# Performance work log

Measured on AMD Instinct MI355X. Metric: run time of the kernel, lower is better.

## Reference

```python
import jax, jax.numpy as jnp
import numpy as np

N = 50000   # nodes
E = 800000  # edges (avg degree 16)
IN, H, OUT = 128, 128, 64


def setup_inputs() -> dict:
    key = jax.random.key(0)
    ks = jax.random.split(key, 8)

    def w(k, shape):
        fan_in = shape[0]
        return (jax.random.normal(k, shape, jnp.float32) / np.float32(np.sqrt(fan_in)))

    x = jax.random.normal(ks[0], (N, IN), jnp.float32)
    edge_index = jax.random.randint(ks[1], (2, E), 0, N, jnp.int64)
    return {
        "x": x,
        "edge_index": edge_index,
        "W1": w(ks[2], (IN, H)), "b1": jnp.zeros((H,), jnp.float32),
        "W2": w(ks[3], (H, H)),  "b2": jnp.zeros((H,), jnp.float32),
        "W3": w(ks[4], (H, H)),  "b3": jnp.zeros((H,), jnp.float32),
        "Wd1": w(ks[5], (H, H)), "bd1": jnp.zeros((H,), jnp.float32),
        "Wd2": w(ks[6], (H, OUT)), "bd2": jnp.zeros((OUT,), jnp.float32),
    }


def _gcn_conv(x, src, dst, norm, W, b):
    # x: [N, Cin] -> linear transform, gather along edges, normalized scatter-add
    h = x @ W                                   # [N, Cout]
    msg = h[src] * norm[:, None]                # [E+N, Cout]
    out = jax.ops.segment_sum(msg, dst, num_segments=N)
    return out + b


def reference(x, edge_index, W1, b1, W2, b2, W3, b3, Wd1, bd1, Wd2, bd2):
    # Add self-loops (PyG GCNConv default) and compute symmetric normalization.
    loops = jnp.arange(N, dtype=edge_index.dtype)
    src = jnp.concatenate([edge_index[0], loops])   # [E+N]
    dst = jnp.concatenate([edge_index[1], loops])   # [E+N]
    deg = jax.ops.segment_sum(jnp.ones_like(dst, dtype=x.dtype), dst, num_segments=N)
    dinv = jnp.where(deg > 0, jax.lax.rsqrt(deg), jnp.zeros_like(deg))
    norm = dinv[src] * dinv[dst]                    # [E+N]

    h = jax.nn.relu(_gcn_conv(x, src, dst, norm, W1, b1))
    h = jax.nn.relu(_gcn_conv(h, src, dst, norm, W2, b2))
    h = jax.nn.relu(_gcn_conv(h, src, dst, norm, W3, b3))

    h = jax.nn.relu(h @ Wd1 + bd1)
    return jax.nn.sigmoid(h @ Wd2 + bd2)            # [N, OUT]
```

## Files before the change

kernel.cpp:

```cpp
#include <hip/hip_runtime.h>
#include <hip/hip_bf16.h>
#include <hip/hip_fp16.h>

#define N_NODES 50000
#define N_EDGES 800000
#define C_H 128
#define C_OUT 64
#define NBLK 196
#define TSTRIDE 136
#define E_PAD 950272
#define MM_BLKS 782

typedef __attribute__((ext_vector_type(8))) short bf16x8;
typedef __attribute__((ext_vector_type(4))) float f32x4;

static __device__ __forceinline__ float bf_lo(unsigned int u) { return __uint_as_float(u << 16); }
static __device__ __forceinline__ float bf_hi(unsigned int u) { return __uint_as_float(u & 0xffff0000u); }
static __device__ __forceinline__ unsigned short f2bf(float f) {
    __hip_bfloat16 h = __float2bfloat16(f);
    return *(unsigned short*)&h;
}
static __device__ __forceinline__ unsigned int pack2(float a, float b) {
    return (unsigned int)f2bf(a) | ((unsigned int)f2bf(b) << 16);
}
static __device__ __forceinline__ unsigned short f2h_bits(float f) {
    union { __half h; unsigned short u; } c; c.h = __float2half_rn(f); return c.u;
}
static __device__ __forceinline__ float h_bits2f(unsigned short u) {
    union { __half h; unsigned short u; } c; c.u = u; return __half2float(c.h);
}

__global__ void prep_kernel(const int* __restrict__ dst, int* __restrict__ counts,
                            int* __restrict__ rank,
                            const float* __restrict__ W1, const float* __restrict__ W2,
                            const float* __restrict__ W3, const float* __restrict__ Wd1,
                            const float* __restrict__ Wd2,
                            unsigned short* __restrict__ P1, unsigned short* __restrict__ P2,
                            unsigned short* __restrict__ P3, unsigned short* __restrict__ Pd1,
                            unsigned short* __restrict__ Pd2,
                            unsigned int* __restrict__ epay) {
    int b = blockIdx.x;
    if (b < 3125) {
        int e = b * 256 + threadIdx.x;
        rank[e] = atomicAdd(&counts[dst[e]], 1);
    } else if (b < 3413) {
        int idx = (b - 3125) * 256 + threadIdx.x;
        if (idx < 4 * 16384) {
            int which = idx >> 14;
            int r = idx & 16383;
            const float* W = (which == 0) ? W1 : (which == 1) ? W2 : (which == 2) ? W3 : Wd1;
            unsigned short* P = (which == 0) ? P1 : (which == 1) ? P2 : (which == 2) ? P3 : Pd1;
            int j = r & 7, lane = (r >> 3) & 63, t = r >> 9;
            int nb = t & 7, kb = t >> 3;
            int k = kb * 32 + ((lane >> 4) << 3) + j;
            int n = nb * 16 + (lane & 15);
            P[r] = f2bf(W[(size_t)k * 128 + n]);
        } else {
            int r = idx - 65536;
            if (r < 8192) {
                int j = r & 7, lane = (r >> 3) & 63, t = r >> 9;
                int nb = t & 3, kb = t >> 2;
                int k = kb * 32 + ((lane >> 4) << 3) + j;
                int n = nb * 16 + (lane & 15);
                Pd2[r] = f2bf(Wd2[(size_t)k * 64 + n]);
            }
        }
    } else {
        int i = (b - 3413) * 256 + threadIdx.x;
        *(uint4*)(epay + (size_t)i * 4) = make_uint4(0, 0, 0, 0);
    }
}

__global__ void __launch_bounds__(256) scan1_kernel(const int* __restrict__ counts,
                                                    int* __restrict__ eblk,
                                                    int* __restrict__ bsum,
                                                    float* __restrict__ dinv) {
    __shared__ int ws[4];
    int i = blockIdx.x * 256 + threadIdx.x;
    int v = (i < N_NODES) ? counts[i] : 0;
    if (i < N_NODES) dinv[i] = rsqrtf((float)v + 1.0f);
    int vp = (v + 3) & ~3;
    int lane = threadIdx.x & 63, w = threadIdx.x >> 6;
    int x = vp;
    #pragma unroll
    for (int off = 1; off < 64; off <<= 1) {
        int t = __shfl_up(x, off, 64);
        if (lane >= off) x += t;
    }
    if (lane == 63) ws[w] = x;
    __syncthreads();
    if (threadIdx.x == 0) {
        int run = 0;
        #pragma unroll
        for (int k = 0; k < 4; ++k) { int t = ws[k]; ws[k] = run; run += t; }
        bsum[blockIdx.x] = run;
    }
    __syncthreads();
    if (i < N_NODES) eblk[i] = x - vp + ws[w];
}

__global__ void __launch_bounds__(256) scan2_kernel(const int* __restrict__ bsum,
                                                    int* __restrict__ bo,
                                                    int* __restrict__ rowptr) {
    __shared__ int ws[4];
    int i = threadIdx.x;
    int v = (i < NBLK) ? bsum[i] : 0;
    int lane = i & 63, w = i >> 6;
    int x = v;
    #pragma unroll
    for (int off = 1; off < 64; off <<= 1) {
        int t = __shfl_up(x, off, 64);
        if (lane >= off) x += t;
    }
    if (lane == 63) ws[w] = x;
    __syncthreads();
    if (i == 0) {
        int run = 0;
        #pragma unroll
        for (int k = 0; k < 4; ++k) { int t = ws[k]; ws[k] = run; run += t; }
    }
    __syncthreads();
    int excl = x - v + ws[w];
    if (i < NBLK) bo[i] = excl;
    if (i == 255) rowptr[N_NODES] = excl + v;
}

__global__ void scan3_kernel(const int* __restrict__ eblk, const int* __restrict__ bo,
                             int* __restrict__ rowptr) {
    int i = blockIdx.x * 256 + threadIdx.x;
    if (i < N_NODES) rowptr[i] = eblk[i] + bo[blockIdx.x];
}

__global__ void __launch_bounds__(256) fill_mm_kernel(
        const float* __restrict__ x, const unsigned short* __restrict__ P1,
        unsigned short* __restrict__ XW1,
        const int* __restrict__ src, const int* __restrict__ dst,
        const float* __restrict__ dinv,
        const int* __restrict__ rowptr, const int* __restrict__ rank,
        unsigned int* __restrict__ epay) {
    int b = blockIdx.x;
    if (b < MM_BLKS) {
        const int lane = threadIdx.x & 63;
        const int wave = threadIdx.x >> 6;
        const int wid  = b * 4 + wave;
        if (wid * 16 >= N_NODES) return;
        const int node = wid * 16 + (lane & 15);
        const int quad = lane >> 4;
        f32x4 acc[8];
        #pragma unroll
        for (int nb = 0; nb < 8; ++nb) acc[nb] = (f32x4){0.f, 0.f, 0.f, 0.f};
        #pragma unroll
        for (int kb = 0; kb < 4; ++kb) {
            const float* p = x + (size_t)node * 128 + kb * 32 + quad * 8;
            float4 lo = *(const float4*)p;
            float4 hi = *(const float4*)(p + 4);
            union { bf16x8 v; unsigned int u[4]; } tmp;
            tmp.u[0] = pack2(lo.x, lo.y); tmp.u[1] = pack2(lo.z, lo.w);
            tmp.u[2] = pack2(hi.x, hi.y); tmp.u[3] = pack2(hi.z, hi.w);
            #pragma unroll
            for (int nb = 0; nb < 8; ++nb) {
                bf16x8 wf = *(const bf16x8*)(P1 + ((size_t)(kb * 8 + nb) * 64 + lane) * 8);
                acc[nb] = __builtin_amdgcn_mfma_f32_16x16x32_bf16(wf, tmp.v, acc[nb], 0, 0, 0);
            }
        }
        #pragma unroll
        for (int nb = 0; nb < 8; ++nb) {
            int ch = nb * 16 + quad * 4;
            uint2 o;
            o.x = pack2(acc[nb][0], acc[nb][1]);
            o.y = pack2(acc[nb][2], acc[nb][3]);
            *(uint2*)(XW1 + (size_t)node * C_H + ch) = o;
        }
    } else {
        int e = (b - MM_BLKS) * 256 + threadIdx.x;
        if (e < N_EDGES) {
            int d = dst[e], s = src[e];
            int pos = rowptr[d] + rank[e];
            float nrm = dinv[s] * dinv[d];
            epay[pos] = (unsigned int)s | ((unsigned int)f2h_bits(nrm) << 16);
        }
    }
}

__global__ void __launch_bounds__(256) gather1_kernel(
        const int* __restrict__ rowptr,
        const unsigned int* __restrict__ epay,
        const float* __restrict__ dinv,
        const unsigned short* __restrict__ hin,
        const float* __restrict__ bias,
        unsigned short* __restrict__ out) {
    int t    = blockIdx.x * 256 + threadIdx.x;
    int node = t >> 4;
    int c8   = (t & 15) << 3;

    float di = dinv[node], dii = di * di;
    uint4 raw = *(const uint4*)(hin + (size_t)node * C_H + c8);
    float a0 = bf_lo(raw.x) * dii, a1 = bf_hi(raw.x) * dii;
    float a2 = bf_lo(raw.y) * dii, a3 = bf_hi(raw.y) * dii;
    float a4 = bf_lo(raw.z) * dii, a5 = bf_hi(raw.z) * dii;
    float a6 = bf_lo(raw.w) * dii, a7 = bf_hi(raw.w) * dii;
    int beg = rowptr[node], end = rowptr[node + 1];
    int p = beg;
    for (; p + 8 <= end; p += 8) {
        uint4 ev0 = *(const uint4*)(epay + p);
        uint4 ev1 = *(const uint4*)(epay + p + 4);
        unsigned int ee[8] = {ev0.x, ev0.y, ev0.z, ev0.w, ev1.x, ev1.y, ev1.z, ev1.w};
        uint4 rv[8];
        #pragma unroll
        for (int j = 0; j < 8; ++j)
            rv[j] = *(const uint4*)(hin + (size_t)(ee[j] & 0xffffu) * C_H + c8);
        #pragma unroll
        for (int j = 0; j < 8; ++j) {
            float nm = h_bits2f((unsigned short)(ee[j] >> 16));
            a0 = fmaf(bf_lo(rv[j].x), nm, a0); a1 = fmaf(bf_hi(rv[j].x), nm, a1);
            a2 = fmaf(bf_lo(rv[j].y), nm, a2); a3 = fmaf(bf_hi(rv[j].y), nm, a3);
            a4 = fmaf(bf_lo(rv[j].z), nm, a4); a5 = fmaf(bf_hi(rv[j].z), nm, a5);
            a6 = fmaf(bf_lo(rv[j].w), nm, a6); a7 = fmaf(bf_hi(rv[j].w), nm, a7);
        }
    }
    if (p < end) {
        uint4 ev = *(const uint4*)(epay + p);
        unsigned int ee[4] = {ev.x, ev.y, ev.z, ev.w};
        uint4 rv[4];
        #pragma unroll
        for (int j = 0; j < 4; ++j)
            rv[j] = *(const uint4*)(hin + (size_t)(ee[j] & 0xffffu) * C_H + c8);
        #pragma unroll
        for (int j = 0; j < 4; ++j) {
            float nm = h_bits2f((unsigned short)(ee[j] >> 16));
            a0 = fmaf(bf_lo(rv[j].x), nm, a0); a1 = fmaf(bf_hi(rv[j].x), nm, a1);
            a2 = fmaf(bf_lo(rv[j].y), nm, a2); a3 = fmaf(bf_hi(rv[j].y), nm, a3);
            a4 = fmaf(bf_lo(rv[j].z), nm, a4); a5 = fmaf(bf_hi(rv[j].z), nm, a5);
            a6 = fmaf(bf_lo(rv[j].w), nm, a6); a7 = fmaf(bf_hi(rv[j].w), nm, a7);
        }
    }
    float4 ba = *(const float4*)(bias + c8);
    float4 bb = *(const float4*)(bias + c8 + 4);
    a0 = fmaxf(a0 + ba.x, 0.f); a1 = fmaxf(a1 + ba.y, 0.f);
    a2 = fmaxf(a2 + ba.z, 0.f); a3 = fmaxf(a3 + ba.w, 0.f);
    a4 = fmaxf(a4 + bb.x, 0.f); a5 = fmaxf(a5 + bb.y, 0.f);
    a6 = fmaxf(a6 + bb.z, 0.f); a7 = fmaxf(a7 + bb.w, 0.f);
    uint4 o;
    o.x = pack2(a0, a1); o.y = pack2(a2, a3);
    o.z = pack2(a4, a5); o.w = pack2(a6, a7);
    *(uint4*)(out + (size_t)node * C_H + c8) = o;
}

template <bool FINAL>
__global__ void __launch_bounds__(256) fused_layer_kernel(
        const int* __restrict__ rowptr,
        const unsigned int* __restrict__ epay,
        const float* __restrict__ dinv,
        const unsigned short* __restrict__ hin,
        const unsigned short* __restrict__ Wp,
        const float* __restrict__ bias,
        const unsigned short* __restrict__ Wd1p,
        const float* __restrict__ bd1,
        const unsigned short* __restrict__ Wd2p,
        const float* __restrict__ bd2,
        unsigned short* __restrict__ out_b,
        float* __restrict__ out_f) {
    __shared__ unsigned short sG[16 * TSTRIDE];
    const int t = threadIdx.x;

    {
        int nl = t >> 4, c8 = (t & 15) << 3;
        int node = blockIdx.x * 16 + nl;
        float di = dinv[node], dii = di * di;
        uint4 raw = *(const uint4*)(hin + (size_t)node * C_H + c8);
        float a0 = bf_lo(raw.x) * dii, a1 = bf_hi(raw.x) * dii;
        float a2 = bf_lo(raw.y) * dii, a3 = bf_hi(raw.y) * dii;
        float a4 = bf_lo(raw.z) * dii, a5 = bf_hi(raw.z) * dii;
        float a6 = bf_lo(raw.w) * dii, a7 = bf_hi(raw.w) * dii;
        int beg = rowptr[node], end = rowptr[node + 1];
        int p = beg;
        for (; p + 8 <= end; p += 8) {
            uint4 ev0 = *(const uint4*)(epay + p);
            uint4 ev1 = *(const uint4*)(epay + p + 4);
            unsigned int ee[8] = {ev0.x, ev0.y, ev0.z, ev0.w, ev1.x, ev1.y, ev1.z, ev1.w};
            uint4 rv[8];
            #pragma unroll
            for (int j = 0; j < 8; ++j)
                rv[j] = *(const uint4*)(hin + (size_t)(ee[j] & 0xffffu) * C_H + c8);
            #pragma unroll
            for (int j = 0; j < 8; ++j) {
                float nm = h_bits2f((unsigned short)(ee[j] >> 16));
                a0 = fmaf(bf_lo(rv[j].x), nm, a0); a1 = fmaf(bf_hi(rv[j].x), nm, a1);
                a2 = fmaf(bf_lo(rv[j].y), nm, a2); a3 = fmaf(bf_hi(rv[j].y), nm, a3);
                a4 = fmaf(bf_lo(rv[j].z), nm, a4); a5 = fmaf(bf_hi(rv[j].z), nm, a5);
                a6 = fmaf(bf_lo(rv[j].w), nm, a6); a7 = fmaf(bf_hi(rv[j].w), nm, a7);
            }
        }
        if (p < end) {
            uint4 ev = *(const uint4*)(epay + p);
            unsigned int ee[4] = {ev.x, ev.y, ev.z, ev.w};
            uint4 rv[4];
            #pragma unroll
            for (int j = 0; j < 4; ++j)
                rv[j] = *(const uint4*)(hin + (size_t)(ee[j] & 0xffffu) * C_H + c8);
            #pragma unroll
            for (int j = 0; j < 4; ++j) {
                float nm = h_bits2f((unsigned short)(ee[j] >> 16));
                a0 = fmaf(bf_lo(rv[j].x), nm, a0); a1 = fmaf(bf_hi(rv[j].x), nm, a1);
                a2 = fmaf(bf_lo(rv[j].y), nm, a2); a3 = fmaf(bf_hi(rv[j].y), nm, a3);
                a4 = fmaf(bf_lo(rv[j].z), nm, a4); a5 = fmaf(bf_hi(rv[j].z), nm, a5);
                a6 = fmaf(bf_lo(rv[j].w), nm, a6); a7 = fmaf(bf_hi(rv[j].w), nm, a7);
            }
        }
        uint4 o;
        o.x = pack2(a0, a1); o.y = pack2(a2, a3);
        o.z = pack2(a4, a5); o.w = pack2(a6, a7);
        *(uint4*)(sG + nl * TSTRIDE + c8) = o;
    }
    __syncthreads();

    const int lane = t & 63, wave = t >> 6, quad = lane >> 4, row = lane & 15;
    const int node = blockIdx.x * 16 + row;

    f32x4 acc0 = (f32x4){0.f, 0.f, 0.f, 0.f};
    f32x4 acc1 = (f32x4){0.f, 0.f, 0.f, 0.f};
    const int nb0 = 2 * wave, nb1 = 2 * wave + 1;
    #pragma unroll
    for (int kb = 0; kb < 4; ++kb) {
        bf16x8 hf = *(const bf16x8*)(sG + row * TSTRIDE + kb * 32 + quad * 8);
        bf16x8 wf0 = *(const bf16x8*)(Wp + ((size_t)(kb * 8 + nb0) * 64 + lane) * 8);
        bf16x8 wf1 = *(const bf16x8*)(Wp + ((size_t)(kb * 8 + nb1) * 64 + lane) * 8);
        acc0 = __builtin_amdgcn_mfma_f32_16x16x32_bf16(wf0, hf, acc0, 0, 0, 0);
        acc1 = __builtin_amdgcn_mfma_f32_16x16x32_bf16(wf1, hf, acc1, 0, 0, 0);
    }
    float4 ba0 = *(const float4*)(bias + nb0 * 16 + quad * 4);
    float4 ba1 = *(const float4*)(bias + nb1 * 16 + quad * 4);
    float v00 = fmaxf(acc0[0] + ba0.x, 0.f), v01 = fmaxf(acc0[1] + ba0.y, 0.f);
    float v02 = fmaxf(acc0[2] + ba0.z, 0.f), v03 = fmaxf(acc0[3] + ba0.w, 0.f);
    float v10 = fmaxf(acc1[0] + ba1.x, 0.f), v11 = fmaxf(acc1[1] + ba1.y, 0.f);
    float v12 = fmaxf(acc1[2] + ba1.z, 0.f), v13 = fmaxf(acc1[3] + ba1.w, 0.f);

    if (!FINAL) {
        uint2 o0, o1;
        o0.x = pack2(v00, v01); o0.y = pack2(v02, v03);
        o1.x = pack2(v10, v11); o1.y = pack2(v12, v13);
        *(uint2*)(out_b + (size_t)node * C_H + nb0 * 16 + quad * 4) = o0;
        *(uint2*)(out_b + (size_t)node * C_H + nb1 * 16 + quad * 4) = o1;
        return;
    }

    __syncthreads();
    {
        uint2 o0, o1;
        o0.x = pack2(v00, v01); o0.y = pack2(v02, v03);
        o1.x = pack2(v10, v11); o1.y = pack2(v12, v13);
        *(uint2*)(sG + row * TSTRIDE + nb0 * 16 + quad * 4) = o0;
        *(uint2*)(sG + row * TSTRIDE + nb1 * 16 + quad * 4) = o1;
    }
    __syncthreads();

    acc0 = (f32x4){0.f, 0.f, 0.f, 0.f};
    acc1 = (f32x4){0.f, 0.f, 0.f, 0.f};
    #pragma unroll
    for (int kb = 0; kb < 4; ++kb) {
        bf16x8 hf = *(const bf16x8*)(sG + row * TSTRIDE + kb * 32 + quad * 8);
        bf16x8 wf0 = *(const bf16x8*)(Wd1p + ((size_t)(kb * 8 + nb0) * 64 + lane) * 8);
        bf16x8 wf1 = *(const bf16x8*)(Wd1p + ((size_t)(kb * 8 + nb1) * 64 + lane) * 8);
        acc0 = __builtin_amdgcn_mfma_f32_16x16x32_bf16(wf0, hf, acc0, 0, 0, 0);
        acc1 = __builtin_amdgcn_mfma_f32_16x16x32_bf16(wf1, hf, acc1, 0, 0, 0);
    }
    ba0 = *(const float4*)(bd1 + nb0 * 16 + quad * 4);
    ba1 = *(const float4*)(bd1 + nb1 * 16 + quad * 4);
    v00 = fmaxf(acc0[0] + ba0.x, 0.f); v01 = fmaxf(acc0[1] + ba0.y, 0.f);
    v02 = fmaxf(acc0[2] + ba0.z, 0.f); v03 = fmaxf(acc0[3] + ba0.w, 0.f);
    v10 = fmaxf(acc1[0] + ba1.x, 0.f); v11 = fmaxf(acc1[1] + ba1.y, 0.f);
    v12 = fmaxf(acc1[2] + ba1.z, 0.f); v13 = fmaxf(acc1[3] + ba1.w, 0.f);
    __syncthreads();
    {
        uint2 o0, o1;
        o0.x = pack2(v00, v01); o0.y = pack2(v02, v03);
        o1.x = pack2(v10, v11); o1.y = pack2(v12, v13);
        *(uint2*)(sG + row * TSTRIDE + nb0 * 16 + quad * 4) = o0;
        *(uint2*)(sG + row * TSTRIDE + nb1 * 16 + quad * 4) = o1;
    }
    __syncthreads();

    f32x4 acc = (f32x4){0.f, 0.f, 0.f, 0.f};
    #pragma unroll
    for (int kb = 0; kb < 4; ++kb) {
        bf16x8 hf = *(const bf16x8*)(sG + row * TSTRIDE + kb * 32 + quad * 8);
        bf16x8 wf = *(const bf16x8*)(Wd2p + ((size_t)(kb * 4 + wave) * 64 + lane) * 8);
        acc = __builtin_amdgcn_mfma_f32_16x16x32_bf16(wf, hf, acc, 0, 0, 0);
    }
    int ch = wave * 16 + quad * 4;
    float4 b4 = *(const float4*)(bd2 + ch);
    float4 r;
    r.x = 1.f / (1.f + expf(-(acc[0] + b4.x)));
    r.y = 1.f / (1.f + expf(-(acc[1] + b4.y)));
    r.z = 1.f / (1.f + expf(-(acc[2] + b4.z)));
    r.w = 1.f / (1.f + expf(-(acc[3] + b4.w)));
    *(float4*)(out_f + (size_t)node * C_OUT + ch) = r;
}

extern "C" void kernel_launch(void* const* d_in, const int* in_sizes, int n_in,
                              void* d_out, int out_size, void* d_ws, size_t ws_size,
                              hipStream_t stream) {
    const float* x   = (const float*)d_in[0];
    const int*   ei  = (const int*)d_in[1];
    const float* W1  = (const float*)d_in[2];
    const float* b1  = (const float*)d_in[3];
    const float* W2  = (const float*)d_in[4];
    const float* b2  = (const float*)d_in[5];
    const float* W3  = (const float*)d_in[6];
    const float* b3  = (const float*)d_in[7];
    const float* Wd1 = (const float*)d_in[8];
    const float* bd1 = (const float*)d_in[9];
    const float* Wd2 = (const float*)d_in[10];
    const float* bd2 = (const float*)d_in[11];

    const int* src = ei;
    const int* dst = ei + N_EDGES;

    char* base = (char*)d_ws;
    size_t off = 0;
    auto alloc = [&](size_t bytes) { char* p = base + off; off += (bytes + 255) & ~size_t(255); return p; };
    int*            counts = (int*)alloc(50176 * 4);
    unsigned int*   epay   = (unsigned int*)alloc((size_t)E_PAD * 4);
    int*            rank   = (int*)alloc((size_t)N_EDGES * 4);
    float*          dinv   = (float*)alloc(N_NODES * 4);
    int*            rowptr = (int*)alloc((N_NODES + 1) * 4);
    int*            eblk   = (int*)alloc(N_NODES * 4);
    int*            bsum   = (int*)alloc(256 * 4);
    int*            bo     = (int*)alloc(256 * 4);
    unsigned short* XW1    = (unsigned short*)alloc((size_t)N_NODES * C_H * 2);
    unsigned short* bufA   = (unsigned short*)alloc((size_t)N_NODES * C_H * 2);
    unsigned short* bufB   = (unsigned short*)alloc((size_t)N_NODES * C_H * 2);
    unsigned short* P1     = (unsigned short*)alloc(128 * 128 * 2);
    unsigned short* P2     = (unsigned short*)alloc(128 * 128 * 2);
    unsigned short* P3     = (unsigned short*)alloc(128 * 128 * 2);
    unsigned short* Pd1    = (unsigned short*)alloc(128 * 128 * 2);
    unsigned short* Pd2    = (unsigned short*)alloc(128 * 64 * 2);

    const int T = 256;
    dim3 blk(T);
    dim3 gN((N_NODES + T - 1) / T);
    dim3 gPrep(3125 + 288 + 928);
    dim3 gFillMM(MM_BLKS + 3125);
    dim3 gFused(N_NODES / 16);

    hipMemsetAsync(counts, 0, 50176 * 4, stream);
    prep_kernel<<<gPrep, blk, 0, stream>>>(dst, counts, rank,
                                           W1, W2, W3, Wd1, Wd2,
                                           P1, P2, P3, Pd1, Pd2, epay);
    scan1_kernel<<<gN, blk, 0, stream>>>(counts, eblk, bsum, dinv);
    scan2_kernel<<<1, blk, 0, stream>>>(bsum, bo, rowptr);
    scan3_kernel<<<gN, blk, 0, stream>>>(eblk, bo, rowptr);
    fill_mm_kernel<<<gFillMM, blk, 0, stream>>>(x, P1, XW1, src, dst, dinv,
                                                rowptr, rank, epay);

    gather1_kernel<<<gFused, blk, 0, stream>>>(rowptr, epay, dinv, XW1, b1, bufA);
    fused_layer_kernel<false><<<gFused, blk, 0, stream>>>(
        rowptr, epay, dinv, bufA, P2, b2, nullptr, nullptr, nullptr, nullptr, bufB, nullptr);
    fused_layer_kernel<true><<<gFused, blk, 0, stream>>>(
        rowptr, epay, dinv, bufB, P3, b3, Pd1, bd1, Pd2, bd2, nullptr, (float*)d_out);
}
```

Baseline: 253.7 us.

## Sort nodes by in-degree bucket to balance gather work per wavefront

Builds a 64-bin histogram of node in-degrees during the scan, computes bucket offsets, and writes a permutation that groups nodes of equal degree. The gather and fused layer kernels then process nodes in permuted order, so the 16 nodes handled by one block have similar edge counts and less divergence. In exchange, node row reads and output writes are no longer contiguous across a block, each kernel adds an indirect perm lookup, and the scan kernels gain shared and global atomics. The memset is widened so it also clears the histogram buffers.

```diff
diff --git a/kernel.cpp b/kernel.cpp
--- a/kernel.cpp
+++ b/kernel.cpp
@@ -74,9 +74,12 @@
 __global__ void __launch_bounds__(256) scan1_kernel(const int* __restrict__ counts,
                                                     int* __restrict__ eblk,
                                                     int* __restrict__ bsum,
-                                                    float* __restrict__ dinv) {
+                                                    float* __restrict__ dinv,
+                                                    int* __restrict__ dhist) {
     __shared__ int ws[4];
+    __shared__ int lh[64];
     int i = blockIdx.x * 256 + threadIdx.x;
+    if (threadIdx.x < 64) lh[threadIdx.x] = 0;
     int v = (i < N_NODES) ? counts[i] : 0;
     if (i < N_NODES) dinv[i] = rsqrtf((float)v + 1.0f);
     int vp = (v + 3) & ~3;
@@ -89,6 +92,7 @@
     }
     if (lane == 63) ws[w] = x;
     __syncthreads();
+    if (i < N_NODES) atomicAdd(&lh[v < 63 ? v : 63], 1);
     if (threadIdx.x == 0) {
         int run = 0;
         #pragma unroll
@@ -97,11 +101,17 @@
     }
     __syncthreads();
     if (i < N_NODES) eblk[i] = x - vp + ws[w];
+    if (threadIdx.x < 64) {
+        int c = lh[threadIdx.x];
+        if (c) atomicAdd(&dhist[threadIdx.x], c);
+    }
 }
 
 __global__ void __launch_bounds__(256) scan2_kernel(const int* __restrict__ bsum,
                                                     int* __restrict__ bo,
-                                                    int* __restrict__ rowptr) {
+                                                    int* __restrict__ rowptr,
+                                                    const int* __restrict__ dhist,
+                                                    int* __restrict__ doff) {
     __shared__ int ws[4];
     int i = threadIdx.x;
     int v = (i < NBLK) ? bsum[i] : 0;
@@ -123,12 +133,42 @@
     int excl = x - v + ws[w];
     if (i < NBLK) bo[i] = excl;
     if (i == 255) rowptr[N_NODES] = excl + v;
+    if (i < 64) {
+        int v2 = dhist[i];
+        int x2 = v2;
+        #pragma unroll
+        for (int off = 1; off < 64; off <<= 1) {
+            int t2 = __shfl_up(x2, off, 64);
+            if (i >= off) x2 += t2;
+        }
+        doff[i] = x2 - v2;
+    }
 }
 
 __global__ void scan3_kernel(const int* __restrict__ eblk, const int* __restrict__ bo,
-                             int* __restrict__ rowptr) {
-    int i = blockIdx.x * 256 + threadIdx.x;
-    if (i < N_NODES) rowptr[i] = eblk[i] + bo[blockIdx.x];
+                             int* __restrict__ rowptr,
+                             const int* __restrict__ counts, int* __restrict__ doff,
+                             int* __restrict__ perm) {
+    __shared__ int lh[64], lbase[64];
+    int tid = threadIdx.x;
+    if (tid < 64) lh[tid] = 0;
+    __syncthreads();
+    int i = blockIdx.x * 256 + tid;
+    int b = 0, r = 0;
+    bool act = (i < N_NODES);
+    if (act) {
+        rowptr[i] = eblk[i] + bo[blockIdx.x];
+        int v = counts[i];
+        b = v < 63 ? v : 63;
+        r = atomicAdd(&lh[b], 1);
+    }
+    __syncthreads();
+    if (tid < 64) {
+        int c = lh[tid];
+        lbase[tid] = c ? atomicAdd(&doff[tid], c) : 0;
+    }
+    __syncthreads();
+    if (act) perm[lbase[b] + r] = i;
 }
 
 __global__ void __launch_bounds__(256) fill_mm_kernel(
@@ -188,9 +228,10 @@
         const float* __restrict__ dinv,
         const unsigned short* __restrict__ hin,
         const float* __restrict__ bias,
-        unsigned short* __restrict__ out) {
+        unsigned short* __restrict__ out,
+        const int* __restrict__ perm) {
     int t    = blockIdx.x * 256 + threadIdx.x;
-    int node = t >> 4;
+    int node = perm[t >> 4];
     int c8   = (t & 15) << 3;
 
     float di = dinv[node], dii = di * di;
@@ -259,13 +300,14 @@
         const unsigned short* __restrict__ Wd2p,
         const float* __restrict__ bd2,
         unsigned short* __restrict__ out_b,
-        float* __restrict__ out_f) {
+        float* __restrict__ out_f,
+        const int* __restrict__ perm) {
     __shared__ unsigned short sG[16 * TSTRIDE];
     const int t = threadIdx.x;
 
     {
         int nl = t >> 4, c8 = (t & 15) << 3;
-        int node = blockIdx.x * 16 + nl;
+        int node = perm[blockIdx.x * 16 + nl];
         float di = dinv[node], dii = di * di;
         uint4 raw = *(const uint4*)(hin + (size_t)node * C_H + c8);
         float a0 = bf_lo(raw.x) * dii, a1 = bf_hi(raw.x) * dii;
@@ -315,7 +357,7 @@
     __syncthreads();
 
     const int lane = t & 63, wave = t >> 6, quad = lane >> 4, row = lane & 15;
-    const int node = blockIdx.x * 16 + row;
+    const int node = perm[blockIdx.x * 16 + row];
 
     f32x4 acc0 = (f32x4){0.f, 0.f, 0.f, 0.f};
     f32x4 acc1 = (f32x4){0.f, 0.f, 0.f, 0.f};
@@ -420,6 +462,8 @@
     size_t off = 0;
     auto alloc = [&](size_t bytes) { char* p = base + off; off += (bytes + 255) & ~size_t(255); return p; };
     int*            counts = (int*)alloc(50176 * 4);
+    int*            dhist  = (int*)alloc(256);
+    int*            doff   = (int*)alloc(256);
     unsigned int*   epay   = (unsigned int*)alloc((size_t)E_PAD * 4);
     int*            rank   = (int*)alloc((size_t)N_EDGES * 4);
     float*          dinv   = (float*)alloc(N_NODES * 4);
@@ -427,6 +471,7 @@
     int*            eblk   = (int*)alloc(N_NODES * 4);
     int*            bsum   = (int*)alloc(256 * 4);
     int*            bo     = (int*)alloc(256 * 4);
+    int*            perm   = (int*)alloc(N_NODES * 4);
     unsigned short* XW1    = (unsigned short*)alloc((size_t)N_NODES * C_H * 2);
     unsigned short* bufA   = (unsigned short*)alloc((size_t)N_NODES * C_H * 2);
     unsigned short* bufB   = (unsigned short*)alloc((size_t)N_NODES * C_H * 2);
@@ -443,19 +488,19 @@
     dim3 gFillMM(MM_BLKS + 3125);
     dim3 gFused(N_NODES / 16);
 
-    hipMemsetAsync(counts, 0, 50176 * 4, stream);
+    hipMemsetAsync(counts, 0, 50176 * 4 + 512, stream);
     prep_kernel<<<gPrep, blk, 0, stream>>>(dst, counts, rank,
                                            W1, W2, W3, Wd1, Wd2,
                                            P1, P2, P3, Pd1, Pd2, epay);
-    scan1_kernel<<<gN, blk, 0, stream>>>(counts, eblk, bsum, dinv);
-    scan2_kernel<<<1, blk, 0, stream>>>(bsum, bo, rowptr);
-    scan3_kernel<<<gN, blk, 0, stream>>>(eblk, bo, rowptr);
+    scan1_kernel<<<gN, blk, 0, stream>>>(counts, eblk, bsum, dinv, dhist);
+    scan2_kernel<<<1, blk, 0, stream>>>(bsum, bo, rowptr, dhist, doff);
+    scan3_kernel<<<gN, blk, 0, stream>>>(eblk, bo, rowptr, counts, doff, perm);
     fill_mm_kernel<<<gFillMM, blk, 0, stream>>>(x, P1, XW1, src, dst, dinv,
                                                 rowptr, rank, epay);
 
-    gather1_kernel<<<gFused, blk, 0, stream>>>(rowptr, epay, dinv, XW1, b1, bufA);
+    gather1_kernel<<<gFused, blk, 0, stream>>>(rowptr, epay, dinv, XW1, b1, bufA, perm);
     fused_layer_kernel<false><<<gFused, blk, 0, stream>>>(
-        rowptr, epay, dinv, bufA, P2, b2, nullptr, nullptr, nullptr, nullptr, bufB, nullptr);
+        rowptr, epay, dinv, bufA, P2, b2, nullptr, nullptr, nullptr, nullptr, bufB, nullptr, perm);
     fused_layer_kernel<true><<<gFused, blk, 0, stream>>>(
-        rowptr, epay, dinv, bufB, P3, b3, Pd1, bd1, Pd2, bd2, nullptr, (float*)d_out);
-}
+        rowptr, epay, dinv, bufB, P3, b3, Pd1, bd1, Pd2, bd2, nullptr, (float*)d_out, perm);
+}
```

Result: no change. 258.7 us (+2.0%).

## Bucket CSR edges by source tile and merge scan kernels

Applied to the files above, without the earlier changes.

Edge ranks are counted per destination and per one of eight source-range tiles, and each node's tile counts are turned into an exclusive prefix. Within each CSR row, edges are then grouped by source range, which should improve locality of the feature-row gathers in the three aggregation layers. The second and third scan kernels are also merged into one launch in which every block redoes the small block-sum scan. In exchange the counter array grows eightfold, so the memset is larger, and the fill step makes an extra counts2 read per edge.

```diff
diff --git a/kernel.cpp b/kernel.cpp
--- a/kernel.cpp
+++ b/kernel.cpp
@@ -10,6 +10,7 @@
 #define TSTRIDE 136
 #define E_PAD 950272
 #define MM_BLKS 782
+#define TILE_N 6250
 
 typedef __attribute__((ext_vector_type(8))) short bf16x8;
 typedef __attribute__((ext_vector_type(4))) float f32x4;
@@ -30,7 +31,8 @@
     union { __half h; unsigned short u; } c; c.u = u; return __half2float(c.h);
 }
 
-__global__ void prep_kernel(const int* __restrict__ dst, int* __restrict__ counts,
+__global__ void prep_kernel(const int* __restrict__ src, const int* __restrict__ dst,
+                            int* __restrict__ counts2,
                             int* __restrict__ rank,
                             const float* __restrict__ W1, const float* __restrict__ W2,
                             const float* __restrict__ W3, const float* __restrict__ Wd1,
@@ -42,7 +44,9 @@
     int b = blockIdx.x;
     if (b < 3125) {
         int e = b * 256 + threadIdx.x;
-        rank[e] = atomicAdd(&counts[dst[e]], 1);
+        int d = dst[e], s = src[e];
+        int t = s / TILE_N;
+        rank[e] = atomicAdd(&counts2[d * 8 + t], 1);
     } else if (b < 3413) {
         int idx = (b - 3125) * 256 + threadIdx.x;
         if (idx < 4 * 16384) {
@@ -71,15 +75,32 @@
     }
 }
 
-__global__ void __launch_bounds__(256) scan1_kernel(const int* __restrict__ counts,
+__global__ void __launch_bounds__(256) scan1_kernel(int* __restrict__ counts2,
                                                     int* __restrict__ eblk,
                                                     int* __restrict__ bsum,
                                                     float* __restrict__ dinv) {
     __shared__ int ws[4];
     int i = blockIdx.x * 256 + threadIdx.x;
-    int v = (i < N_NODES) ? counts[i] : 0;
-    if (i < N_NODES) dinv[i] = rsqrtf((float)v + 1.0f);
-    int vp = (v + 3) & ~3;
+    int deg = 0;
+    if (i < N_NODES) {
+        int* c = counts2 + (size_t)i * 8;
+        uint4 a = *(uint4*)c;
+        uint4 bq = *(uint4*)(c + 4);
+        int run = 0, tv;
+        tv = a.x;  a.x  = run; run += tv;
+        tv = a.y;  a.y  = run; run += tv;
+        tv = a.z;  a.z  = run; run += tv;
+        tv = a.w;  a.w  = run; run += tv;
+        tv = bq.x; bq.x = run; run += tv;
+        tv = bq.y; bq.y = run; run += tv;
+        tv = bq.z; bq.z = run; run += tv;
+        tv = bq.w; bq.w = run; run += tv;
+        deg = run;
+        *(uint4*)c = a;
+        *(uint4*)(c + 4) = bq;
+        dinv[i] = rsqrtf((float)deg + 1.0f);
+    }
+    int vp = (deg + 3) & ~3;
     int lane = threadIdx.x & 63, w = threadIdx.x >> 6;
     int x = vp;
     #pragma unroll
@@ -99,10 +120,11 @@
     if (i < N_NODES) eblk[i] = x - vp + ws[w];
 }
 
-__global__ void __launch_bounds__(256) scan2_kernel(const int* __restrict__ bsum,
-                                                    int* __restrict__ bo,
+__global__ void __launch_bounds__(256) scanB_kernel(const int* __restrict__ eblk,
+                                                    const int* __restrict__ bsum,
                                                     int* __restrict__ rowptr) {
     __shared__ int ws[4];
+    __shared__ int sbo;
     int i = threadIdx.x;
     int v = (i < NBLK) ? bsum[i] : 0;
     int lane = i & 63, w = i >> 6;
@@ -121,14 +143,11 @@
     }
     __syncthreads();
     int excl = x - v + ws[w];
-    if (i < NBLK) bo[i] = excl;
-    if (i == 255) rowptr[N_NODES] = excl + v;
-}
-
-__global__ void scan3_kernel(const int* __restrict__ eblk, const int* __restrict__ bo,
-                             int* __restrict__ rowptr) {
-    int i = blockIdx.x * 256 + threadIdx.x;
-    if (i < N_NODES) rowptr[i] = eblk[i] + bo[blockIdx.x];
+    if (i == (int)blockIdx.x) sbo = excl;
+    if (blockIdx.x == 0 && i == NBLK - 1) rowptr[N_NODES] = excl + v;
+    __syncthreads();
+    int g = blockIdx.x * 256 + threadIdx.x;
+    if (g < N_NODES) rowptr[g] = eblk[g] + sbo;
 }
 
 __global__ void __launch_bounds__(256) fill_mm_kernel(
@@ -136,7 +155,8 @@
         unsigned short* __restrict__ XW1,
         const int* __restrict__ src, const int* __restrict__ dst,
         const float* __restrict__ dinv,
-        const int* __restrict__ rowptr, const int* __restrict__ rank,
+        const int* __restrict__ rowptr, const int* __restrict__ counts2,
+        const int* __restrict__ rank,
         unsigned int* __restrict__ epay) {
     int b = blockIdx.x;
     if (b < MM_BLKS) {
@@ -175,7 +195,8 @@
         int e = (b - MM_BLKS) * 256 + threadIdx.x;
         if (e < N_EDGES) {
             int d = dst[e], s = src[e];
-            int pos = rowptr[d] + rank[e];
+            int t = s / TILE_N;
+            int pos = rowptr[d] + counts2[d * 8 + t] + rank[e];
             float nrm = dinv[s] * dinv[d];
             epay[pos] = (unsigned int)s | ((unsigned int)f2h_bits(nrm) << 16);
         }
@@ -419,14 +440,13 @@
     char* base = (char*)d_ws;
     size_t off = 0;
     auto alloc = [&](size_t bytes) { char* p = base + off; off += (bytes + 255) & ~size_t(255); return p; };
-    int*            counts = (int*)alloc(50176 * 4);
+    int*            counts2 = (int*)alloc((size_t)N_NODES * 8 * 4);
     unsigned int*   epay   = (unsigned int*)alloc((size_t)E_PAD * 4);
     int*            rank   = (int*)alloc((size_t)N_EDGES * 4);
     float*          dinv   = (float*)alloc(N_NODES * 4);
     int*            rowptr = (int*)alloc((N_NODES + 1) * 4);
     int*            eblk   = (int*)alloc(N_NODES * 4);
     int*            bsum   = (int*)alloc(256 * 4);
-    int*            bo     = (int*)alloc(256 * 4);
     unsigned short* XW1    = (unsigned short*)alloc((size_t)N_NODES * C_H * 2);
     unsigned short* bufA   = (unsigned short*)alloc((size_t)N_NODES * C_H * 2);
     unsigned short* bufB   = (unsigned short*)alloc((size_t)N_NODES * C_H * 2);
@@ -443,15 +463,14 @@
     dim3 gFillMM(MM_BLKS + 3125);
     dim3 gFused(N_NODES / 16);
 
-    hipMemsetAsync(counts, 0, 50176 * 4, stream);
-    prep_kernel<<<gPrep, blk, 0, stream>>>(dst, counts, rank,
+    hipMemsetAsync(counts2, 0, (size_t)N_NODES * 8 * 4, stream);
+    prep_kernel<<<gPrep, blk, 0, stream>>>(src, dst, counts2, rank,
                                            W1, W2, W3, Wd1, Wd2,
                                            P1, P2, P3, Pd1, Pd2, epay);
-    scan1_kernel<<<gN, blk, 0, stream>>>(counts, eblk, bsum, dinv);
-    scan2_kernel<<<1, blk, 0, stream>>>(bsum, bo, rowptr);
-    scan3_kernel<<<gN, blk, 0, stream>>>(eblk, bo, rowptr);
+    scan1_kernel<<<gN, blk, 0, stream>>>(counts2, eblk, bsum, dinv);
+    scanB_kernel<<<gN, blk, 0, stream>>>(eblk, bsum, rowptr);
     fill_mm_kernel<<<gFillMM, blk, 0, stream>>>(x, P1, XW1, src, dst, dinv,
-                                                rowptr, rank, epay);
+                                                rowptr, counts2, rank, epay);
 
     gather1_kernel<<<gFused, blk, 0, stream>>>(rowptr, epay, dinv, XW1, b1, bufA);
     fused_layer_kernel<false><<<gFused, blk, 0, stream>>>(
```

Result: no change. 252.7 us (median of 2 runs) (-0.4%).
